# Kernel optimization log

Hardware: AMD Instinct MI355X
Metric: run time of the kernel (lower is better)

Reference implementation:

```python
import jax, jax.numpy as jnp
import numpy as np

PRIOR = 0.2
TEMP = 1.0
THRESHOLD = 0.5
B, L, D, H = 8, 4096, 768, 512


def setup_inputs() -> dict:
    key = jax.random.key(0)
    k1, k2, k3, k4 = jax.random.split(key, 4)
    hidden = jax.random.normal(k1, (B, L, D), jnp.float32)
    # MLP params: Linear(D,H) -> ReLU -> Linear(H,1)
    W1 = jax.random.normal(k2, (D, H), jnp.float32) / np.sqrt(D).astype(np.float32)
    b1 = jnp.zeros((H,), jnp.float32)
    W2 = jax.random.normal(k3, (H, 1), jnp.float32) / np.sqrt(H).astype(np.float32)
    b2 = jnp.zeros((1,), jnp.float32)
    # pre-sampled uniform noise for the RelaxedBernoulli logistic reparameterization
    noise_u = jax.random.uniform(k4, (B, L), jnp.float32, minval=1e-6, maxval=1.0 - 1e-6)
    return dict(hidden=hidden, W1=W1, b1=b1, W2=W2, b2=b2, noise_u=noise_u)


def reference(hidden, W1, b1, W2, b2, noise_u):
    bs, seq_len, model_dim = hidden.shape
    # boundary MLP -> per-token logits [B, L]
    h = jax.nn.relu(jnp.einsum('bld,dh->blh', hidden, W1) + b1)
    logits = (jnp.einsum('blh,ho->blo', h, W2) + b2)[..., 0]
    # RelaxedBernoulli rsample: sigmoid((logits + logistic_noise) / temp),
    # since logit(sigmoid(logits)) == logits
    logistic_noise = jnp.log(noise_u) - jnp.log1p(-noise_u)
    soft_boundaries = jax.nn.sigmoid((logits + logistic_noise) / TEMP)
    hard_bin = (soft_boundaries > THRESHOLD).astype(soft_boundaries.dtype)
    # straight-through estimator
    hard_boundaries = soft_boundaries + jax.lax.stop_gradient(hard_bin - soft_boundaries)
    # segment id of each token: number of boundaries strictly before it
    # (boundary token is the last element of its segment)
    seg = (jnp.cumsum(hard_bin, axis=1) - hard_bin).astype(jnp.int32)  # [B, L] in [0, L)
    ids = (seg + seq_len * jnp.arange(bs, dtype=jnp.int32)[:, None]).reshape(-1)
    flat = hidden.reshape(bs * seq_len, model_dim)
    seg_sum = jax.ops.segment_sum(flat, ids, num_segments=bs * seq_len)
    seg_cnt = jax.ops.segment_sum(jnp.ones((bs * seq_len,), hidden.dtype), ids,
                                  num_segments=bs * seq_len)
    # mean pooling per segment; unused segment slots stay zero (padded to L segments,
    # equivalent to the torch [S,B,D]->transpose output up to zero padding)
    pooled = (seg_sum / jnp.maximum(seg_cnt, 1.0)[:, None]).reshape(bs, seq_len, model_dim)
    # hinge loss on boundary rate: penalize |rate - (prior+0.05)| beyond margin 0.05
    ratio = jnp.mean(hard_boundaries)
    loss = jax.nn.relu(jnp.abs(ratio - (PRIOR + 0.05)) - 0.05)
    num_boundaries = jnp.sum(hard_bin)
    total_positions = jnp.asarray(bs * seq_len, jnp.float32)
    return pooled, loss, num_boundaries, total_positions
```

## Files before the change

kernel.cpp:

```cpp
#include <hip/hip_runtime.h>
#include <math.h>

typedef __attribute__((ext_vector_type(8))) short short8;
typedef __attribute__((ext_vector_type(4))) float float4v;
typedef unsigned int uint;

#define BATCH 8
#define SEQ   4096
#define DIM   768
#define HID   512
#define M_TOK (BATCH * SEQ)

static __device__ __forceinline__ short f2bf_rne(float x) {
    unsigned int u = __float_as_uint(x);
    unsigned int r = (u + 0x7FFFu + ((u >> 16) & 1u)) >> 16;
    return (short)r;
}
static __device__ __forceinline__ uint pack_bf2(float a, float b) {
    return __builtin_amdgcn_perm(__float_as_uint(b), __float_as_uint(a), 0x07060302u);
}
union FragU { uint u[4]; short8 s; };
static __device__ __forceinline__ void gl2lds16(const void* g, void* l) {
    __builtin_amdgcn_global_load_lds(
        (const __attribute__((address_space(1))) unsigned int*)g,
        (__attribute__((address_space(3))) unsigned int*)l, 16, 0, 0);
}

__global__ __launch_bounds__(256) void prep_kernel(const float* __restrict__ W1,
                                                   short* __restrict__ W1T) {
    __shared__ float t[64][65];
    const int bk = blockIdx.x % 12, bn = blockIdx.x / 12;
    const int k0 = bk * 64, n0 = bn * 64;
    const int tr = threadIdx.x >> 6, tc = threadIdx.x & 63;
#pragma unroll
    for (int i = 0; i < 16; i++) {
        int k = tr + i * 4;
        t[k][tc] = W1[(size_t)(k0 + k) * HID + n0 + tc];
    }
    __syncthreads();
#pragma unroll
    for (int i = 0; i < 16; i++) {
        int n = tr + i * 4;
        W1T[(size_t)(n0 + n) * DIM + k0 + tc] = f2bf_rne(t[tc][n]);
    }
}

#define MLP_BM    128
#define MLP_STEPS 24
#define MLP_ABYTES 16384
#define MLP_BBYTES 32768
#define MLP_BUF   (MLP_ABYTES + MLP_BBYTES)
#define MLP_LDS   (3 * MLP_BUF)

__global__ __launch_bounds__(512, 2) void mlp_kernel(const float* __restrict__ A,
                                                     const short* __restrict__ BT,
                                                     const float* __restrict__ b1,
                                                     const float* __restrict__ W2,
                                                     float* __restrict__ logits) {
    extern __shared__ char smem[];
    const int tid = threadIdx.x, wave = tid >> 6, lane = tid & 63;
    const int q = lane >> 4, r = lane & 15;
    const int wr = wave >> 2, wc = wave & 3;
    const int m0 = blockIdx.x * MLP_BM;

    const float* aS0 = A + (size_t)(m0 + wave * 16 + r) * DIM + q * 8;
    const float* aS1 = aS0 + 4;
    const int aD0 = wave * 2048, aD1 = wave * 2048 + 1024;
    const short* bS[4];
    int bD[4];
#pragma unroll
    for (int j = 0; j < 4; j++) {
        int h = wave * 4 + j;
        bS[j] = BT + (size_t)(h * 16 + r) * DIM + q * 8;
        bD[j] = MLP_ABYTES + h * 1024;
    }

    float4v acc[4][8] = {};

    auto stage = [&](int t, char* nb) {
        const int ko = t * 32;
        gl2lds16(aS0 + ko, nb + aD0);
        gl2lds16(aS1 + ko, nb + aD1);
#pragma unroll
        for (int j = 0; j < 4; j++) gl2lds16(bS[j] + ko, nb + bD[j]);
    };
    auto compute = [&](const char* base) {
        short8 bfr[8];
#pragma unroll
        for (int nf = 0; nf < 8; nf++)
            bfr[nf] = *(const short8*)(base + MLP_ABYTES + (wc * 8 + nf) * 1024 + lane * 16);
#pragma unroll
        for (int mf = 0; mf < 4; mf++) {
            const int g = wr * 4 + mf;
            float4v f0 = *(const float4v*)(base + g * 2048 + lane * 16);
            float4v f1 = *(const float4v*)(base + g * 2048 + 1024 + lane * 16);
            FragU af;
            af.u[0] = pack_bf2(f0[0], f0[1]);
            af.u[1] = pack_bf2(f0[2], f0[3]);
            af.u[2] = pack_bf2(f1[0], f1[1]);
            af.u[3] = pack_bf2(f1[2], f1[3]);
#pragma unroll
            for (int nf = 0; nf < 8; nf++)
                acc[mf][nf] = __builtin_amdgcn_mfma_f32_16x16x32_bf16(
                    af.s, bfr[nf], acc[mf][nf], 0, 0, 0);
        }
    };

    stage(0, smem);
    stage(1, smem + MLP_BUF);
    stage(2, smem + 2 * MLP_BUF);

    for (int t = 0; t <= MLP_STEPS - 4; ++t) {
        asm volatile("s_waitcnt vmcnt(12)" ::: "memory");
        __builtin_amdgcn_s_barrier();
        __builtin_amdgcn_sched_barrier(0);
        compute(smem + (t % 3) * MLP_BUF);
        __builtin_amdgcn_sched_barrier(0);
        __builtin_amdgcn_s_barrier();
        stage(t + 3, smem + (t % 3) * MLP_BUF);
    }
    asm volatile("s_waitcnt vmcnt(12)" ::: "memory");
    __builtin_amdgcn_s_barrier();
    __builtin_amdgcn_sched_barrier(0);
    compute(smem + ((MLP_STEPS - 3) % 3) * MLP_BUF);
    __builtin_amdgcn_sched_barrier(0);
    asm volatile("s_waitcnt vmcnt(6)" ::: "memory");
    __builtin_amdgcn_s_barrier();
    __builtin_amdgcn_sched_barrier(0);
    compute(smem + ((MLP_STEPS - 2) % 3) * MLP_BUF);
    __builtin_amdgcn_sched_barrier(0);
    asm volatile("s_waitcnt vmcnt(0)" ::: "memory");
    __builtin_amdgcn_s_barrier();
    __builtin_amdgcn_sched_barrier(0);
    compute(smem + ((MLP_STEPS - 1) % 3) * MLP_BUF);

    float b1v[8], w2v[8];
#pragma unroll
    for (int nf = 0; nf < 8; nf++) {
        int gc = wc * 128 + nf * 16 + r;
        b1v[nf] = b1[gc];
        w2v[nf] = W2[gc];
    }
    float* red = (float*)smem;
#pragma unroll
    for (int mf = 0; mf < 4; mf++)
#pragma unroll
        for (int v = 0; v < 4; v++) {
            float pp = 0.f;
#pragma unroll
            for (int nf = 0; nf < 8; nf++) {
                float hh = acc[mf][nf][v] + b1v[nf];
                hh = hh > 0.f ? hh : 0.f;
                pp += hh * w2v[nf];
            }
#pragma unroll
            for (int off = 1; off < 16; off <<= 1) pp += __shfl_xor(pp, off, 64);
            if (r == 0) red[wc * 128 + wr * 64 + mf * 16 + q * 4 + v] = pp;
        }
    __syncthreads();
    if (tid < 128) {
        logits[m0 + tid] = red[tid] + red[128 + tid] + red[256 + tid] + red[384 + tid];
    }
}

__global__ __launch_bounds__(1024) void boundary_kernel(const float* __restrict__ logits,
                                                        const float* __restrict__ b2p,
                                                        const float* __restrict__ noise,
                                                        int* __restrict__ starts,
                                                        int* __restrict__ nseg,
                                                        int* __restrict__ nbcount) {
    const int b = blockIdx.x, tid = threadIdx.x;
    const int base = tid * 4;
    const float b2 = b2p[0];
    int h[4], c = 0;
#pragma unroll
    for (int j = 0; j < 4; j++) {
        int l = base + j;
        float u = noise[b * SEQ + l];
        float lg = logits[b * SEQ + l] + b2 + logf(u) - log1pf(-u);
        h[j] = (lg > 0.f) ? 1 : 0;
        c += h[j];
    }
    const int lane = tid & 63, wid = tid >> 6;
    int inc = c;
    for (int off = 1; off < 64; off <<= 1) {
        int t = __shfl_up(inc, off, 64);
        if (lane >= off) inc += t;
    }
    __shared__ int wtot[16], woff[16], extra[2];
    if (lane == 63) wtot[wid] = inc;
    if (tid == 1023) extra[0] = h[3];
    __syncthreads();
    if (tid == 0) {
        int s = 0;
        for (int i = 0; i < 16; i++) { woff[i] = s; s += wtot[i]; }
        extra[1] = s;
    }
    __syncthreads();
    int run = (inc - c) + woff[wid];
#pragma unroll
    for (int j = 0; j < 4; j++) {
        int l = base + j;
        if (h[j]) {
            run++;
            if (l < SEQ - 1) starts[b * (SEQ + 1) + run] = l + 1;
        }
    }
    if (tid == 0) {
        int total = extra[1];
        int ns = total + (extra[0] ? 0 : 1);
        starts[b * (SEQ + 1)] = 0;
        starts[b * (SEQ + 1) + ns] = SEQ;
        nseg[b] = ns;
        nbcount[b] = total;
    }
}

__global__ __launch_bounds__(256) void pool_kernel(const float* __restrict__ hidden,
                                                   const int* __restrict__ starts,
                                                   const int* __restrict__ nseg,
                                                   float* __restrict__ out) {
    const int wid = threadIdx.x >> 6, lane = threadIdx.x & 63;
    const int s = blockIdx.x * 4 + wid, b = blockIdx.y;
    float* orow = out + (size_t)(b * SEQ + s) * DIM;
    float4v a0 = {0.f, 0.f, 0.f, 0.f}, a1 = a0, a2 = a0;
    const int ns = nseg[b];
    if (s < ns) {
        const int st = starts[b * (SEQ + 1) + s];
        const int en = starts[b * (SEQ + 1) + s + 1];
        float4v c0 = a0, c1 = a0, c2 = a0;
        const float* hbase = hidden + (size_t)(b * SEQ) * DIM;
        int row = st;
        for (; row + 2 <= en; row += 2) {
            const float* h0 = hbase + (size_t)row * DIM;
            const float* h1 = h0 + DIM;
            a0 += *(const float4v*)(h0 + lane * 4);
            a1 += *(const float4v*)(h0 + (lane + 64) * 4);
            a2 += *(const float4v*)(h0 + (lane + 128) * 4);
            c0 += *(const float4v*)(h1 + lane * 4);
            c1 += *(const float4v*)(h1 + (lane + 64) * 4);
            c2 += *(const float4v*)(h1 + (lane + 128) * 4);
        }
        if (row < en) {
            const float* h0 = hbase + (size_t)row * DIM;
            a0 += *(const float4v*)(h0 + lane * 4);
            a1 += *(const float4v*)(h0 + (lane + 64) * 4);
            a2 += *(const float4v*)(h0 + (lane + 128) * 4);
        }
        a0 += c0; a1 += c1; a2 += c2;
        const float invc = 1.f / (float)(en - st);
        a0 *= invc; a1 *= invc; a2 *= invc;
    }
    __builtin_nontemporal_store(a0, (float4v*)(orow + lane * 4));
    __builtin_nontemporal_store(a1, (float4v*)(orow + (lane + 64) * 4));
    __builtin_nontemporal_store(a2, (float4v*)(orow + (lane + 128) * 4));
}

__global__ void finalize_kernel(const int* __restrict__ nbcount, float* __restrict__ tail) {
    int nb = 0;
    for (int i = 0; i < BATCH; i++) nb += nbcount[i];
    float ratio = (float)nb / (float)M_TOK;
    float d = fabsf(ratio - 0.25f) - 0.05f;
    tail[0] = d > 0.f ? d : 0.f;
    tail[1] = (float)nb;
    tail[2] = (float)M_TOK;
}

extern "C" void kernel_launch(void* const* d_in, const int* in_sizes, int n_in,
                              void* d_out, int out_size, void* d_ws, size_t ws_size,
                              hipStream_t stream) {
    const float* hidden = (const float*)d_in[0];
    const float* W1     = (const float*)d_in[1];
    const float* b1     = (const float*)d_in[2];
    const float* W2     = (const float*)d_in[3];
    const float* b2     = (const float*)d_in[4];
    const float* noise  = (const float*)d_in[5];

    char* ws = (char*)d_ws;
    short* W1T    = (short*)(ws);
    float* logits = (float*)(ws + 786432);
    int*   starts = (int*)(ws + 917504);
    int*   nseg   = (int*)(ws + 917504 + 131104);
    int*   nbcount = nseg + 8;
    float* out    = (float*)d_out;

    static bool s_mlp_attr = false;
    if (!s_mlp_attr) {
        hipFuncSetAttribute(reinterpret_cast<const void*>(mlp_kernel),
                            hipFuncAttributeMaxDynamicSharedMemorySize, MLP_LDS);
        s_mlp_attr = true;
    }

    prep_kernel<<<96, 256, 0, stream>>>(W1, W1T);
    mlp_kernel<<<M_TOK / MLP_BM, 512, MLP_LDS, stream>>>(hidden, W1T, b1, W2, logits);
    boundary_kernel<<<BATCH, 1024, 0, stream>>>(logits, b2, noise, starts, nseg, nbcount);
    pool_kernel<<<dim3(SEQ / 4, BATCH), 256, 0, stream>>>(hidden, starts, nseg, out);
    finalize_kernel<<<1, 1, 0, stream>>>(nbcount, out + (size_t)M_TOK * DIM);
}
```

Before: 233.6 us.

## Prefetch LDS fragments into registers before MFMA cluster and raise wave priority

```diff
diff --git a/kernel.cpp b/kernel.cpp
--- a/kernel.cpp
+++ b/kernel.cpp
@@ -76,6 +76,8 @@
     }
 
     float4v acc[4][8] = {};
+    FragU aF[4];
+    short8 bF[8];
 
     auto stage = [&](int t, char* nb) {
         const int ko = t * 32;
@@ -84,55 +86,77 @@
 #pragma unroll
         for (int j = 0; j < 4; j++) gl2lds16(bS[j] + ko, nb + bD[j]);
     };
-    auto compute = [&](const char* base) {
-        short8 bfr[8];
+    auto loadFrags = [&](const char* base) {
 #pragma unroll
         for (int nf = 0; nf < 8; nf++)
-            bfr[nf] = *(const short8*)(base + MLP_ABYTES + (wc * 8 + nf) * 1024 + lane * 16);
+            bF[nf] = *(const short8*)(base + MLP_ABYTES + (wc * 8 + nf) * 1024 + lane * 16);
 #pragma unroll
         for (int mf = 0; mf < 4; mf++) {
             const int g = wr * 4 + mf;
             float4v f0 = *(const float4v*)(base + g * 2048 + lane * 16);
             float4v f1 = *(const float4v*)(base + g * 2048 + 1024 + lane * 16);
-            FragU af;
-            af.u[0] = pack_bf2(f0[0], f0[1]);
-            af.u[1] = pack_bf2(f0[2], f0[3]);
-            af.u[2] = pack_bf2(f1[0], f1[1]);
-            af.u[3] = pack_bf2(f1[2], f1[3]);
+            aF[mf].u[0] = pack_bf2(f0[0], f0[1]);
+            aF[mf].u[1] = pack_bf2(f0[2], f0[3]);
+            aF[mf].u[2] = pack_bf2(f1[0], f1[1]);
+            aF[mf].u[3] = pack_bf2(f1[2], f1[3]);
+        }
+    };
+    auto mfmaClus = [&]() {
+#pragma unroll
+        for (int mf = 0; mf < 4; mf++)
 #pragma unroll
             for (int nf = 0; nf < 8; nf++)
                 acc[mf][nf] = __builtin_amdgcn_mfma_f32_16x16x32_bf16(
-                    af.s, bfr[nf], acc[mf][nf], 0, 0, 0);
-        }
-    };
-
-    stage(0, smem);
-    stage(1, smem + MLP_BUF);
-    stage(2, smem + 2 * MLP_BUF);
-
-    for (int t = 0; t <= MLP_STEPS - 4; ++t) {
-        asm volatile("s_waitcnt vmcnt(12)" ::: "memory");
+                    aF[mf].s, bF[nf], acc[mf][nf], 0, 0, 0);
+    };
+    auto computePhase = [&]() {
+        __builtin_amdgcn_sched_barrier(0);
+        __builtin_amdgcn_s_setprio(1);
+        mfmaClus();
+        __builtin_amdgcn_s_setprio(0);
+        __builtin_amdgcn_sched_barrier(0);
+    };
+    auto loadPhase = [&](const char* base) {
         __builtin_amdgcn_s_barrier();
-        __builtin_amdgcn_sched_barrier(0);
-        compute(smem + (t % 3) * MLP_BUF);
+        loadFrags(base);
+        asm volatile("s_waitcnt lgkmcnt(0)" ::: "memory");
         __builtin_amdgcn_sched_barrier(0);
         __builtin_amdgcn_s_barrier();
-        stage(t + 3, smem + (t % 3) * MLP_BUF);
-    }
+    };
+
+    char* buf0 = smem;
+    char* buf1 = smem + MLP_BUF;
+    char* buf2 = smem + 2 * MLP_BUF;
+
+    stage(0, buf0);
+    stage(1, buf1);
+    stage(2, buf2);
     asm volatile("s_waitcnt vmcnt(12)" ::: "memory");
-    __builtin_amdgcn_s_barrier();
-    __builtin_amdgcn_sched_barrier(0);
-    compute(smem + ((MLP_STEPS - 3) % 3) * MLP_BUF);
-    __builtin_amdgcn_sched_barrier(0);
-    asm volatile("s_waitcnt vmcnt(6)" ::: "memory");
-    __builtin_amdgcn_s_barrier();
-    __builtin_amdgcn_sched_barrier(0);
-    compute(smem + ((MLP_STEPS - 2) % 3) * MLP_BUF);
-    __builtin_amdgcn_sched_barrier(0);
-    asm volatile("s_waitcnt vmcnt(0)" ::: "memory");
-    __builtin_amdgcn_s_barrier();
-    __builtin_amdgcn_sched_barrier(0);
-    compute(smem + ((MLP_STEPS - 1) % 3) * MLP_BUF);
+    loadPhase(buf0);
+
+    for (int tb = 0; tb < 18; tb += 6) {
+#pragma unroll
+        for (int j = 0; j < 6; j++) {
+            const int t = tb + j;
+            char* sb = (j % 3 == 0) ? buf0 : (j % 3 == 1) ? buf1 : buf2;
+            char* lb = ((j + 1) % 3 == 0) ? buf0 : ((j + 1) % 3 == 1) ? buf1 : buf2;
+            stage(t + 3, sb);
+            computePhase();
+            asm volatile("s_waitcnt vmcnt(12)" ::: "memory");
+            loadPhase(lb);
+        }
+    }
+    stage(21, buf0); computePhase();
+    asm volatile("s_waitcnt vmcnt(12)" ::: "memory"); loadPhase(buf1);
+    stage(22, buf1); computePhase();
+    asm volatile("s_waitcnt vmcnt(12)" ::: "memory"); loadPhase(buf2);
+    stage(23, buf2); computePhase();
+    asm volatile("s_waitcnt vmcnt(12)" ::: "memory"); loadPhase(buf0);
+    computePhase();
+    asm volatile("s_waitcnt vmcnt(6)" ::: "memory");  loadPhase(buf1);
+    computePhase();
+    asm volatile("s_waitcnt vmcnt(0)" ::: "memory");  loadPhase(buf2);
+    computePhase();
 
     float b1v[8], w2v[8];
 #pragma unroll
```

New measurement: 236.2 us. Within noise of the previous version (+1.1%).

## Shrink MLP tile to 64 rows with 4 waves and double buffering

Applied to the files above, without the earlier changes.

```diff
diff --git a/kernel.cpp b/kernel.cpp
--- a/kernel.cpp
+++ b/kernel.cpp
@@ -45,14 +45,14 @@
     }
 }
 
-#define MLP_BM    128
+#define MLP_BM    64
 #define MLP_STEPS 24
-#define MLP_ABYTES 16384
+#define MLP_ABYTES 8192
 #define MLP_BBYTES 32768
 #define MLP_BUF   (MLP_ABYTES + MLP_BBYTES)
-#define MLP_LDS   (3 * MLP_BUF)
-
-__global__ __launch_bounds__(512, 2) void mlp_kernel(const float* __restrict__ A,
+#define MLP_LDS   (2 * MLP_BUF)
+
+__global__ __launch_bounds__(256, 2) void mlp_kernel(const float* __restrict__ A,
                                                      const short* __restrict__ BT,
                                                      const float* __restrict__ b1,
                                                      const float* __restrict__ W2,
@@ -60,17 +60,16 @@
     extern __shared__ char smem[];
     const int tid = threadIdx.x, wave = tid >> 6, lane = tid & 63;
     const int q = lane >> 4, r = lane & 15;
-    const int wr = wave >> 2, wc = wave & 3;
     const int m0 = blockIdx.x * MLP_BM;
 
     const float* aS0 = A + (size_t)(m0 + wave * 16 + r) * DIM + q * 8;
     const float* aS1 = aS0 + 4;
     const int aD0 = wave * 2048, aD1 = wave * 2048 + 1024;
-    const short* bS[4];
-    int bD[4];
-#pragma unroll
-    for (int j = 0; j < 4; j++) {
-        int h = wave * 4 + j;
+    const short* bS[8];
+    int bD[8];
+#pragma unroll
+    for (int j = 0; j < 8; j++) {
+        int h = wave * 8 + j;
         bS[j] = BT + (size_t)(h * 16 + r) * DIM + q * 8;
         bD[j] = MLP_ABYTES + h * 1024;
     }
@@ -82,18 +81,17 @@
         gl2lds16(aS0 + ko, nb + aD0);
         gl2lds16(aS1 + ko, nb + aD1);
 #pragma unroll
-        for (int j = 0; j < 4; j++) gl2lds16(bS[j] + ko, nb + bD[j]);
+        for (int j = 0; j < 8; j++) gl2lds16(bS[j] + ko, nb + bD[j]);
     };
     auto compute = [&](const char* base) {
         short8 bfr[8];
 #pragma unroll
         for (int nf = 0; nf < 8; nf++)
-            bfr[nf] = *(const short8*)(base + MLP_ABYTES + (wc * 8 + nf) * 1024 + lane * 16);
+            bfr[nf] = *(const short8*)(base + MLP_ABYTES + (wave * 8 + nf) * 1024 + lane * 16);
 #pragma unroll
         for (int mf = 0; mf < 4; mf++) {
-            const int g = wr * 4 + mf;
-            float4v f0 = *(const float4v*)(base + g * 2048 + lane * 16);
-            float4v f1 = *(const float4v*)(base + g * 2048 + 1024 + lane * 16);
+            float4v f0 = *(const float4v*)(base + mf * 2048 + lane * 16);
+            float4v f1 = *(const float4v*)(base + mf * 2048 + 1024 + lane * 16);
             FragU af;
             af.u[0] = pack_bf2(f0[0], f0[1]);
             af.u[1] = pack_bf2(f0[2], f0[3]);
@@ -106,41 +104,45 @@
         }
     };
 
-    stage(0, smem);
-    stage(1, smem + MLP_BUF);
-    stage(2, smem + 2 * MLP_BUF);
-
-    for (int t = 0; t <= MLP_STEPS - 4; ++t) {
-        asm volatile("s_waitcnt vmcnt(12)" ::: "memory");
+    char* buf0 = smem;
+    char* buf1 = smem + MLP_BUF;
+
+    stage(0, buf0);
+    stage(1, buf1);
+
+    for (int tb = 0; tb < 22; tb += 2) {
+        asm volatile("s_waitcnt vmcnt(10)" ::: "memory");
         __builtin_amdgcn_s_barrier();
         __builtin_amdgcn_sched_barrier(0);
-        compute(smem + (t % 3) * MLP_BUF);
+        compute(buf0);
         __builtin_amdgcn_sched_barrier(0);
         __builtin_amdgcn_s_barrier();
-        stage(t + 3, smem + (t % 3) * MLP_BUF);
-    }
-    asm volatile("s_waitcnt vmcnt(12)" ::: "memory");
+        stage(tb + 2, buf0);
+        asm volatile("s_waitcnt vmcnt(10)" ::: "memory");
+        __builtin_amdgcn_s_barrier();
+        __builtin_amdgcn_sched_barrier(0);
+        compute(buf1);
+        __builtin_amdgcn_sched_barrier(0);
+        __builtin_amdgcn_s_barrier();
+        stage(tb + 3, buf1);
+    }
+    asm volatile("s_waitcnt vmcnt(10)" ::: "memory");
     __builtin_amdgcn_s_barrier();
     __builtin_amdgcn_sched_barrier(0);
-    compute(smem + ((MLP_STEPS - 3) % 3) * MLP_BUF);
-    __builtin_amdgcn_sched_barrier(0);
-    asm volatile("s_waitcnt vmcnt(6)" ::: "memory");
-    __builtin_amdgcn_s_barrier();
-    __builtin_amdgcn_sched_barrier(0);
-    compute(smem + ((MLP_STEPS - 2) % 3) * MLP_BUF);
-    __builtin_amdgcn_sched_barrier(0);
+    compute(buf0);
     asm volatile("s_waitcnt vmcnt(0)" ::: "memory");
     __builtin_amdgcn_s_barrier();
     __builtin_amdgcn_sched_barrier(0);
-    compute(smem + ((MLP_STEPS - 1) % 3) * MLP_BUF);
+    compute(buf1);
 
     float b1v[8], w2v[8];
 #pragma unroll
     for (int nf = 0; nf < 8; nf++) {
-        int gc = wc * 128 + nf * 16 + r;
+        int gc = wave * 128 + nf * 16 + r;
         b1v[nf] = b1[gc];
         w2v[nf] = W2[gc];
     }
+    __syncthreads();
     float* red = (float*)smem;
 #pragma unroll
     for (int mf = 0; mf < 4; mf++)
@@ -155,11 +157,11 @@
             }
 #pragma unroll
             for (int off = 1; off < 16; off <<= 1) pp += __shfl_xor(pp, off, 64);
-            if (r == 0) red[wc * 128 + wr * 64 + mf * 16 + q * 4 + v] = pp;
-        }
-    __syncthreads();
-    if (tid < 128) {
-        logits[m0 + tid] = red[tid] + red[128 + tid] + red[256 + tid] + red[384 + tid];
+            if (r == 0) red[wave * 64 + mf * 16 + q * 4 + v] = pp;
+        }
+    __syncthreads();
+    if (tid < 64) {
+        logits[m0 + tid] = red[tid] + red[64 + tid] + red[128 + tid] + red[192 + tid];
     }
 }
 
@@ -292,7 +294,7 @@
     }
 
     prep_kernel<<<96, 256, 0, stream>>>(W1, W1T);
-    mlp_kernel<<<M_TOK / MLP_BM, 512, MLP_LDS, stream>>>(hidden, W1T, b1, W2, logits);
+    mlp_kernel<<<M_TOK / MLP_BM, 256, MLP_LDS, stream>>>(hidden, W1T, b1, W2, logits);
     boundary_kernel<<<BATCH, 1024, 0, stream>>>(logits, b2, noise, starts, nseg, nbcount);
     pool_kernel<<<dim3(SEQ / 4, BATCH), 256, 0, stream>>>(hidden, starts, nseg, out);
     finalize_kernel<<<1, 1, 0, stream>>>(nbcount, out + (size_t)M_TOK * DIM);
```

Measured after the change: 252.6 us. 8.1% more time.
